# Kernel optimization log

Hardware: AMD Instinct MI355X
Metric: run time of the kernel (lower is better)

The kernel has to match this reference:

```python
import jax, jax.numpy as jnp
import numpy as np

N_QUBITS = 12
DIM = 2 ** N_QUBITS
BATCH = 2048


def setup_inputs() -> dict:
    key = jax.random.key(0)
    k1, k2, k3 = jax.random.split(key, 3)
    inputs = jax.random.normal(k1, (BATCH, N_QUBITS), dtype=jnp.float32)
    weight = jax.random.normal(k2, (3 + 2 * N_QUBITS,), dtype=jnp.float32)
    entangle_matrix = jax.random.normal(k3, (DIM, DIM), dtype=jnp.float32)
    return {"inputs": inputs, "weight": weight, "entangle_matrix": entangle_matrix}


def _encode(ry_angles, rz_angles):
    # Encoder: state = prod over qubits of first column of (Rz*Ry) per qubit.
    ry = ry_angles / 2
    rz = rz_angles / 2
    a = jnp.cos(ry) * jnp.exp(-1j * rz)  # entry11 (row bit = 0)
    b = jnp.sin(ry) * jnp.exp(1j * rz)   # entry21 (row bit = 1)
    col2 = jnp.stack([a, b], axis=-1).astype(jnp.complex64)  # [B, n, 2]
    B, n = ry.shape
    v = jnp.ones((B, 1), dtype=jnp.complex64)
    for q in range(n):  # Kronecker fold over qubits (big-endian, matches dec2bin)
        v = (v[:, :, None] * col2[:, q][:, None, :]).reshape(B, -1)
    return v  # [B, 2^n]


def _rot_mat(w):
    # rot_mat: per-qubit Rx(w[q]) @ Rz(w[n+q]), then full Kronecker product.
    n = w.shape[0] // 2
    tx = (w[:n] / 2).astype(jnp.complex64)
    tz = (w[n:] / 2).astype(jnp.complex64)
    c, s = jnp.cos(tx), jnp.sin(tx)
    rx = jnp.stack([jnp.stack([c, -1j * s], -1),
                    jnp.stack([-1j * s, c], -1)], -2)  # [n,2,2]
    ez = jnp.exp(-1j * tz)
    zero = jnp.zeros_like(ez)
    rz = jnp.stack([jnp.stack([ez, zero], -1),
                    jnp.stack([zero, jnp.exp(1j * tz)], -1)], -2)  # [n,2,2]
    mats = jnp.einsum('qij,qjk->qik', rx, rz)
    M = mats[0]
    for q in range(1, n):
        M = jnp.kron(M, mats[q])
    return M  # [2^n, 2^n]


def _ry2(theta):
    a = theta / 2
    c, s = jnp.cos(a), jnp.sin(a)
    return jnp.stack([jnp.stack([c, -s]), jnp.stack([s, c])])  # [2,2] real


def _final_rot(th3):
    # final_rot_mat: Rz-form @ Ry-form @ Rx-form (all ry_mat_list), kron with identity.
    rot = _ry2(th3[2]) @ (_ry2(th3[1]) @ _ry2(th3[0]))
    eye = jnp.eye(DIM // 2, dtype=jnp.complex64)
    return jnp.kron(rot.astype(jnp.complex64), eye)  # [DIM, DIM]


def reference(inputs, weight, entangle_matrix):
    # initial=False branch
    ry_angles = inputs
    rz_angles = jnp.square(inputs)
    v = _encode(ry_angles, rz_angles)                 # [B, DIM] complex64
    E = entangle_matrix.astype(jnp.complex64)
    R = _rot_mat(weight[3:])
    M = E @ R @ E                                     # [DIM, DIM]
    v = v @ M.T                                       # tensordot dims ([-1],[-1])
    F = _final_rot(weight[:3])
    v = v @ F.T
    half = DIM // 2
    # vector[:, half:] = 0 then sum |.|^2  <=>  sum over first half
    return jnp.sum(jnp.square(jnp.abs(v[:, :half])), axis=-1)  # [B] float32
```

## Files before the change

### kernel.cpp

```cpp
#include <hip/hip_runtime.h>
#include <math.h>

#define QDIM 4096
#define NQ 12
#define QBATCH 2048

typedef _Float16 f16x8 __attribute__((ext_vector_type(8)));
typedef float f32x4 __attribute__((ext_vector_type(4)));
typedef int i32x4 __attribute__((ext_vector_type(4)));

__device__ __forceinline__ void gld_lds16(const void* gptr, void* ldsptr) {
    __builtin_amdgcn_global_load_lds(
        (const __attribute__((address_space(1))) void*)gptr,
        (__attribute__((address_space(3))) void*)ldsptr,
        16, 0, 0);
}

__device__ __forceinline__ int q8(float x) {
    float y = fminf(fmaxf(x, -127.f), 127.f);
    return (int)rintf(y);
}
__device__ __forceinline__ int pack4_i8(int a, int b, int c, int d) {
    return (a & 0xFF) | ((b & 0xFF) << 8) | ((c & 0xFF) << 16) | ((d & 0xFF) << 24);
}

__global__ __launch_bounds__(256) void conv_kernel(
    const float* __restrict__ E, const float* __restrict__ wgt,
    _Float16* __restrict__ Eh, signed char* __restrict__ G8)
{
    float th = 0.5f * (wgt[0] + wgt[1] + wgt[2]);
    float c0 = cosf(th), c1 = -sinf(th);
    const float qs = 127.f / 6.f;
    size_t flat = ((size_t)blockIdx.x * 256 + threadIdx.x) * 8;
    size_t n = flat >> 12;
    size_t k = flat & (QDIM - 1);
    const float* p0 = E + n * QDIM + k;
    const float* p1 = p0 + (size_t)QBATCH * QDIM;
    float4 a0 = ((const float4*)p0)[0], a1 = ((const float4*)p0)[1];
    float4 b0 = ((const float4*)p1)[0], b1 = ((const float4*)p1)[1];
    f16x8 h0 = { (_Float16)a0.x, (_Float16)a0.y, (_Float16)a0.z, (_Float16)a0.w,
                 (_Float16)a1.x, (_Float16)a1.y, (_Float16)a1.z, (_Float16)a1.w };
    f16x8 h1 = { (_Float16)b0.x, (_Float16)b0.y, (_Float16)b0.z, (_Float16)b0.w,
                 (_Float16)b1.x, (_Float16)b1.y, (_Float16)b1.z, (_Float16)b1.w };
    *(f16x8*)&Eh[n * QDIM + k] = h0;
    *(f16x8*)&Eh[(n + QBATCH) * QDIM + k] = h1;
    float g[8] = { c0*a0.x + c1*b0.x, c0*a0.y + c1*b0.y, c0*a0.z + c1*b0.z, c0*a0.w + c1*b0.w,
                   c0*a1.x + c1*b1.x, c0*a1.y + c1*b1.y, c0*a1.z + c1*b1.z, c0*a1.w + c1*b1.w };
    int2 gp = { pack4_i8(q8(g[0]*qs), q8(g[1]*qs), q8(g[2]*qs), q8(g[3]*qs)),
                pack4_i8(q8(g[4]*qs), q8(g[5]*qs), q8(g[6]*qs), q8(g[7]*qs)) };
    *(int2*)&G8[n * QDIM + k] = gp;
}

__global__ __launch_bounds__(256) void expand_kernel(
    const float* __restrict__ inputs, _Float16* __restrict__ A1,
    float* __restrict__ out)
{
    __shared__ float ab[NQ][4];
    const int b = blockIdx.x;
    const int tid = threadIdx.x;
    if (tid == 0) out[b] = 0.f;
    if (tid < NQ) {
        float x = inputs[b * NQ + tid];
        float ry = 0.5f * x;
        float rz = 0.5f * x * x;
        float ca = cosf(ry), sa = sinf(ry), cz = cosf(rz), sz = sinf(rz);
        ab[tid][0] = ca * cz;  ab[tid][1] = -ca * sz;
        ab[tid][2] = sa * cz;  ab[tid][3] =  sa * sz;
    }
    __syncthreads();
    float pr0 = 1.f, pi0 = 0.f;
#pragma unroll
    for (int q = 0; q < 8; ++q) {
        int bit = (tid >> (7 - q)) & 1;
        float cr = ab[q][bit * 2 + 0], ci = ab[q][bit * 2 + 1];
        float nr = pr0 * cr - pi0 * ci;
        float ni = pr0 * ci + pi0 * cr;
        pr0 = nr; pi0 = ni;
    }
    f16x8 vr[2], vi[2];
#pragma unroll
    for (int u = 0; u < 16; ++u) {
        float pr = pr0, pi = pi0;
#pragma unroll
        for (int q = 8; q < 12; ++q) {
            int bit = (u >> (11 - q)) & 1;
            float cr = ab[q][bit * 2 + 0], ci = ab[q][bit * 2 + 1];
            float nr = pr * cr - pi * ci;
            float ni = pr * ci + pi * cr;
            pr = nr; pi = ni;
        }
        vr[u >> 3][u & 7] = (_Float16)pr;
        vi[u >> 3][u & 7] = (_Float16)pi;
    }
    const int idx0 = tid * 16;
    *(f16x8*)&A1[(size_t)b * QDIM + idx0] = vr[0];
    *(f16x8*)&A1[(size_t)b * QDIM + idx0 + 8] = vr[1];
    *(f16x8*)&A1[(size_t)(b + QBATCH) * QDIM + idx0] = vi[0];
    *(f16x8*)&A1[(size_t)(b + QBATCH) * QDIM + idx0 + 8] = vi[1];
}

#define VMCNT(N_) asm volatile("s_waitcnt vmcnt(" #N_ ")" ::: "memory")
#define LGKM0()   asm volatile("s_waitcnt lgkmcnt(0)" ::: "memory")
#define LGKM8()   asm volatile("s_waitcnt lgkmcnt(8)" ::: "memory")
#define SBAR()                              \
    do {                                    \
        asm volatile("" ::: "memory");      \
        __builtin_amdgcn_s_barrier();       \
        asm volatile("" ::: "memory");      \
    } while (0)

__global__ __launch_bounds__(512, 2) void gemm_f16_256(
    const _Float16* __restrict__ A, const _Float16* __restrict__ B,
    _Float16* __restrict__ C, int N)
{
    const int K = QDIM;
    __shared__ __attribute__((aligned(16))) _Float16 As[2][256 * 64];
    __shared__ __attribute__((aligned(16))) _Float16 Bs[2][256 * 64];

    const int tid  = threadIdx.x;
    const int wave = tid >> 6;
    const int lane = tid & 63;
    const int bm0 = blockIdx.y * 256;
    const int bn0 = blockIdx.x * 256;
    const int wm0 = (wave >> 2) * 128;
    const int wn0 = (wave & 3) * 64;
    const int q = lane >> 4;
    const int r = lane & 15;
    const int rx = r & 7;

    f32x4 acc[8][4];
#pragma unroll
    for (int i = 0; i < 8; ++i)
#pragma unroll
        for (int j = 0; j < 4; ++j) acc[i][j] = (f32x4){0.f, 0.f, 0.f, 0.f};

    const int srow = tid >> 3;
    const int scol = ((tid & 7) ^ (srow & 7)) * 8;
    const _Float16* gA = A + (size_t)(bm0 + srow) * K + scol;
    const _Float16* gB = B + (size_t)(bn0 + srow) * K + scol;

#define STG_A(D, KK, NN) gld_lds16(gA + (size_t)(NN) * 64 * K + (KK), &As[D][(NN) * 4096 + wave * 512])
#define STG_B(D, KK, NN) gld_lds16(gB + (size_t)(NN) * 64 * K + (KK), &Bs[D][(NN) * 4096 + wave * 512])
#define STG_AH(D, KK, H) do { STG_A(D, KK, 2*(H)); STG_A(D, KK, 2*(H)+1); } while (0)
#define STG_BH(D, KK, H) do { STG_B(D, KK, 2*(H)); STG_B(D, KK, 2*(H)+1); } while (0)

#define RD_A4(DST, D, IB)                                                          \
    _Pragma("unroll")                                                              \
    for (int ii = 0; ii < 4; ++ii) {                                               \
        _Pragma("unroll")                                                          \
        for (int ss = 0; ss < 2; ++ss)                                             \
            DST[ii][ss] = *(const f16x8*)&As[D][(wm0 + ((IB) + ii) * 16 + r) * 64  \
                                                + (((ss * 4 + q) ^ rx) * 8)];      \
    }
#define RD_B2(DST, D, JB)                                                          \
    _Pragma("unroll")                                                              \
    for (int jj = 0; jj < 2; ++jj) {                                               \
        _Pragma("unroll")                                                          \
        for (int ss = 0; ss < 2; ++ss)                                             \
            DST[jj][ss] = *(const f16x8*)&Bs[D][(wn0 + ((JB) + jj) * 16 + r) * 64  \
                                                + (((ss * 4 + q) ^ rx) * 8)];      \
    }
#define MM8(AR, BR, I0, J0)                                                        \
    _Pragma("unroll")                                                              \
    for (int ii = 0; ii < 4; ++ii) {                                               \
        _Pragma("unroll")                                                          \
        for (int jj = 0; jj < 2; ++jj) {                                           \
            acc[(I0) + ii][(J0) + jj] = __builtin_amdgcn_mfma_f32_16x16x32_f16(    \
                AR[ii][0], BR[jj][0], acc[(I0) + ii][(J0) + jj], 0, 0, 0);         \
            acc[(I0) + ii][(J0) + jj] = __builtin_amdgcn_mfma_f32_16x16x32_f16(    \
                AR[ii][1], BR[jj][1], acc[(I0) + ii][(J0) + jj], 0, 0, 0);         \
        }                                                                          \
    }

    f16x8 a0[4][2], a1[4][2], b0[2][2], b1[2][2];

    STG_AH(0, 0, 0); STG_AH(0, 0, 1);
    STG_BH(0, 0, 0); STG_BH(0, 0, 1);
    STG_BH(1, 64, 0); STG_BH(1, 64, 1);
    VMCNT(4);
    SBAR();

    for (int tau = 0; tau < 32; ++tau) {
        const int k1 = (2 * tau + 1) * 64;
        const int k2 = ((2 * tau + 2) & 63) * 64;
        const int k3 = ((2 * tau + 3) & 63) * 64;

        RD_A4(a0, 0, 0); RD_B2(b0, 0, 0);
        STG_AH(1, k1, 0);
        LGKM8();
        SBAR(); LGKM0();
        __builtin_amdgcn_s_setprio(1);
        MM8(a0, b0, 0, 0);
        __builtin_amdgcn_s_setprio(0);
        SBAR();

        RD_B2(b1, 0, 2);
        STG_AH(1, k1, 1);
        SBAR(); LGKM0();
        __builtin_amdgcn_s_setprio(1);
        MM8(a0, b1, 0, 2);
        __builtin_amdgcn_s_setprio(0);
        SBAR();

        RD_A4(a1, 0, 4);
        STG_BH(0, k2, 0);
        SBAR(); LGKM0();
        __builtin_amdgcn_s_setprio(1);
        MM8(a1, b1, 4, 2);
        __builtin_amdgcn_s_setprio(0);
        SBAR();

        STG_BH(0, k2, 1);
        VMCNT(4);
        SBAR(); LGKM0();
        __builtin_amdgcn_s_setprio(1);
        MM8(a1, b0, 4, 0);
        __builtin_amdgcn_s_setprio(0);
        SBAR();

        RD_A4(a0, 1, 0); RD_B2(b0, 1, 0);
        STG_AH(0, k2, 0);
        LGKM8();
        SBAR(); LGKM0();
        __builtin_amdgcn_s_setprio(1);
        MM8(a0, b0, 0, 0);
        __builtin_amdgcn_s_setprio(0);
        SBAR();

        RD_B2(b1, 1, 2);
        STG_AH(0, k2, 1);
        SBAR(); LGKM0();
        __builtin_amdgcn_s_setprio(1);
        MM8(a0, b1, 0, 2);
        __builtin_amdgcn_s_setprio(0);
        SBAR();

        RD_A4(a1, 1, 4);
        STG_BH(1, k3, 0);
        SBAR(); LGKM0();
        __builtin_amdgcn_s_setprio(1);
        MM8(a1, b1, 4, 2);
        __builtin_amdgcn_s_setprio(0);
        SBAR();

        STG_BH(1, k3, 1);
        VMCNT(4);
        SBAR(); LGKM0();
        __builtin_amdgcn_s_setprio(1);
        MM8(a1, b0, 4, 0);
        __builtin_amdgcn_s_setprio(0);
        SBAR();
    }
    VMCNT(0);

#pragma unroll
    for (int i = 0; i < 8; ++i) {
        const int crow = bm0 + wm0 + i * 16 + q * 4;
#pragma unroll
        for (int rr = 0; rr < 4; ++rr)
#pragma unroll
            for (int j = 0; j < 4; ++j)
                C[(size_t)(crow + rr) * N + bn0 + wn0 + j * 16 + r] = (_Float16)acc[i][j][rr];
    }
#undef STG_A
#undef STG_B
#undef STG_AH
#undef STG_BH
#undef RD_A4
#undef RD_B2
#undef MM8
}

__global__ __launch_bounds__(256) void butterfly_kernel(
    const _Float16* __restrict__ u1, const float* __restrict__ wgt,
    signed char* __restrict__ A2, float* __restrict__ scaleA)
{
    __shared__ float sRe[4366];
    __shared__ float sIm[4366];
    __shared__ float mats[NQ][8];
    __shared__ float red[8];
    const int blk = blockIdx.x;
    const int tid = threadIdx.x;
    const int ah = tid >> 4;
    const int al = tid & 15;

    if (tid < NQ) {
        float tx = 0.5f * wgt[3 + tid];
        float tz = 0.5f * wgt[15 + tid];
        float c = cosf(tx), s = sinf(tx), cz = cosf(tz), sz = sinf(tz);
        mats[tid][0] =  c * cz;  mats[tid][1] = -c * sz;
        mats[tid][2] =  s * sz;  mats[tid][3] = -s * cz;
        mats[tid][4] = -s * sz;  mats[tid][5] = -s * cz;
        mats[tid][6] =  c * cz;  mats[tid][7] =  c * sz;
    }

    float xr[16], xi[16];
    {
        const _Float16* pRe = u1 + (size_t)blk * QDIM + tid * 16;
        const _Float16* pIm = u1 + (size_t)(blk + QBATCH) * QDIM + tid * 16;
        f16x8 r0 = ((const f16x8*)pRe)[0], r1 = ((const f16x8*)pRe)[1];
        f16x8 i0 = ((const f16x8*)pIm)[0], i1 = ((const f16x8*)pIm)[1];
#pragma unroll
        for (int j = 0; j < 8; ++j) {
            xr[j] = (float)r0[j]; xr[8 + j] = (float)r1[j];
            xi[j] = (float)i0[j]; xi[8 + j] = (float)i1[j];
        }
    }
    __syncthreads();

#define BFLY_STAGE(arrR, arrI, K_, Q_)                                         \
    {                                                                          \
        const float m00r = mats[Q_][0], m00i = mats[Q_][1];                    \
        const float m01r = mats[Q_][2], m01i = mats[Q_][3];                    \
        const float m10r = mats[Q_][4], m10i = mats[Q_][5];                    \
        const float m11r = mats[Q_][6], m11i = mats[Q_][7];                    \
        _Pragma("unroll")                                                      \
        for (int t = 0; t < 8; ++t) {                                          \
            int i0 = ((t >> (K_)) << ((K_) + 1)) | (t & ((1 << (K_)) - 1));    \
            int i1 = i0 | (1 << (K_));                                         \
            float x0r = arrR[i0], x0i = arrI[i0];                              \
            float x1r = arrR[i1], x1i = arrI[i1];                              \
            arrR[i0] = m00r * x0r - m00i * x0i + m01r * x1r - m01i * x1i;      \
            arrI[i0] = m00r * x0i + m00i * x0r + m01r * x1i + m01i * x1r;      \
            arrR[i1] = m10r * x0r - m10i * x0i + m11r * x1r - m11i * x1i;      \
            arrI[i1] = m10r * x0i + m10i * x0r + m11r * x1i + m11i * x1r;      \
        }                                                                      \
    }

#pragma unroll
    for (int p = 0; p < 4; ++p) BFLY_STAGE(xr, xi, p, 11 - p);

#pragma unroll
    for (int c = 0; c < 16; ++c) {
        sRe[273 * ah + 17 * al + c] = xr[c];
        sIm[273 * ah + 17 * al + c] = xi[c];
    }
    __syncthreads();

    float yr[16], yi[16];
#pragma unroll
    for (int b = 0; b < 16; ++b) {
        yr[b] = sRe[273 * ah + 17 * b + al];
        yi[b] = sIm[273 * ah + 17 * b + al];
    }
#pragma unroll
    for (int p = 0; p < 4; ++p) BFLY_STAGE(yr, yi, p, 7 - p);

#pragma unroll
    for (int b = 0; b < 16; ++b) {
        sRe[273 * ah + 17 * b + al] = yr[b];
        sIm[273 * ah + 17 * b + al] = yi[b];
    }
    __syncthreads();

    float zr[16], zi[16];
#pragma unroll
    for (int a = 0; a < 16; ++a) {
        zr[a] = sRe[273 * a + 17 * ah + al];
        zi[a] = sIm[273 * a + 17 * ah + al];
    }
#pragma unroll
    for (int p = 0; p < 4; ++p) BFLY_STAGE(zr, zi, p, 3 - p);

    float mR = 0.f, mI = 0.f;
#pragma unroll
    for (int j = 0; j < 16; ++j) {
        mR = fmaxf(mR, fabsf(zr[j]));
        mI = fmaxf(mI, fabsf(zi[j]));
    }
#pragma unroll
    for (int off = 32; off > 0; off >>= 1) {
        mR = fmaxf(mR, __shfl_xor(mR, off, 64));
        mI = fmaxf(mI, __shfl_xor(mI, off, 64));
    }
    const int wid = tid >> 6;
    if ((tid & 63) == 0) { red[wid] = mR; red[4 + wid] = mI; }
    __syncthreads();
    mR = fmaxf(fmaxf(red[0], red[1]), fmaxf(red[2], red[3]));
    mI = fmaxf(fmaxf(red[4], red[5]), fmaxf(red[6], red[7]));
    mR = fmaxf(mR, 1e-30f);
    mI = fmaxf(mI, 1e-30f);
    if (tid == 0) {
        scaleA[blk] = mR / 127.f;
        scaleA[blk + QBATCH] = mI / 127.f;
    }
    const float invR = 127.f / mR, invI = 127.f / mI;

    signed char* oRe = A2 + (size_t)blk * QDIM + ah * 16 + al;
    signed char* oIm = A2 + (size_t)(blk + QBATCH) * QDIM + ah * 16 + al;
#pragma unroll
    for (int a = 0; a < 16; ++a) {
        oRe[a * 256] = (signed char)q8(zr[a] * invR);
        oIm[a * 256] = (signed char)q8(zi[a] * invI);
    }
#undef BFLY_STAGE
}

__global__ __launch_bounds__(256) void gemm2_i8(
    const signed char* __restrict__ A, const signed char* __restrict__ B,
    const float* __restrict__ scaleA, float* __restrict__ out)
{
    const int K = QDIM;
    __shared__ __attribute__((aligned(16))) signed char As[128 * 128];
    __shared__ __attribute__((aligned(16))) signed char Bs[128 * 128];

    const int tid  = threadIdx.x;
    const int wave = tid >> 6;
    const int lane = tid & 63;
    const int bn0 = blockIdx.x * 128;
    const int bm0 = blockIdx.y * 128;
    const int wm = (wave >> 1) * 64;
    const int wn = (wave & 1) * 64;
    const int q = lane >> 4;
    const int r = lane & 15;
    const int rx = r & 7;

    i32x4 acc[4][4];
#pragma unroll
    for (int i = 0; i < 4; ++i)
#pragma unroll
        for (int j = 0; j < 4; ++j) acc[i][j] = (i32x4){0, 0, 0, 0};

    const signed char* gA[4];
    const signed char* gB[4];
    char* lA[4];
    char* lB[4];
#pragma unroll
    for (int n = 0; n < 4; ++n) {
        int c = n * 256 + tid;
        int row = c >> 3;
        int gcol = (c & 7) ^ (row & 7);
        gA[n] = A + (size_t)(bm0 + row) * K + gcol * 16;
        gB[n] = B + (size_t)(bn0 + row) * K + gcol * 16;
        lA[n] = (char*)As + (n * 256 + wave * 64) * 16;
        lB[n] = (char*)Bs + (n * 256 + wave * 64) * 16;
    }

    for (int kk = 0; kk < K; kk += 128) {
#pragma unroll
        for (int n = 0; n < 4; ++n) {
            gld_lds16(gA[n] + kk, lA[n]);
            gld_lds16(gB[n] + kk, lB[n]);
        }
        __syncthreads();

#pragma unroll
        for (int s = 0; s < 2; ++s) {
            i32x4 af[4], bf[4];
#pragma unroll
            for (int i = 0; i < 4; ++i) {
                int row = wm + i * 16 + r;
                af[i] = *(const i32x4*)&As[row * 128 + (((s * 4 + q) ^ rx) * 16)];
            }
#pragma unroll
            for (int j = 0; j < 4; ++j) {
                int row = wn + j * 16 + r;
                bf[j] = *(const i32x4*)&Bs[row * 128 + (((s * 4 + q) ^ rx) * 16)];
            }
#pragma unroll
            for (int i = 0; i < 4; ++i)
#pragma unroll
                for (int j = 0; j < 4; ++j)
                    acc[i][j] = __builtin_amdgcn_mfma_i32_16x16x64_i8(af[i], bf[j], acc[i][j], 0, 0, 0);
        }
        __syncthreads();
    }

    const float dqG = 6.f / 127.f;
#pragma unroll
    for (int i = 0; i < 4; ++i) {
#pragma unroll
        for (int rr = 0; rr < 4; ++rr) {
            const int row = bm0 + wm + i * 16 + q * 4 + rr;
            const float sc = scaleA[row] * dqG;
            float v = 0.f;
#pragma unroll
            for (int j = 0; j < 4; ++j) {
                float t = sc * (float)acc[i][j][rr];
                v = fmaf(t, t, v);
            }
            v += __shfl_xor(v, 1, 64);
            v += __shfl_xor(v, 2, 64);
            v += __shfl_xor(v, 4, 64);
            v += __shfl_xor(v, 8, 64);
            if (r == 0) atomicAdd(&out[row & (QBATCH - 1)], v);
        }
    }
}

extern "C" void kernel_launch(void* const* d_in, const int* in_sizes, int n_in,
                              void* d_out, int out_size, void* d_ws, size_t ws_size,
                              hipStream_t stream)
{
    const float* inputs = (const float*)d_in[0];
    const float* weight = (const float*)d_in[1];
    const float* E      = (const float*)d_in[2];
    float* out = (float*)d_out;

    char* ws = (char*)d_ws;
    const size_t MB = 1024 * 1024;
    _Float16*    Eh     = (_Float16*)   (ws + 0);
    signed char* G8     = (signed char*)(ws + 32 * MB);
    _Float16*    A1     = (_Float16*)   (ws + 40 * MB);
    _Float16*    u1     = (_Float16*)   (ws + 72 * MB);
    signed char* A2     = (signed char*)(ws + 104 * MB);
    float*       scaleA = (float*)      (ws + 120 * MB);

    conv_kernel<<<(QBATCH * QDIM / 8) / 256, 256, 0, stream>>>(E, weight, Eh, G8);
    expand_kernel<<<QBATCH, 256, 0, stream>>>(inputs, A1, out);
    gemm_f16_256<<<dim3(QDIM / 256, QDIM / 256), 512, 0, stream>>>(A1, Eh, u1, QDIM);
    butterfly_kernel<<<QBATCH, 256, 0, stream>>>(u1, weight, A2, scaleA);
    gemm2_i8<<<dim3(2048 / 128, QDIM / 128), 256, 0, stream>>>(A2, G8, scaleA, out);
}
```

Measured before the change: 299.0 us.

## Software-pipeline LDS fragment reads one phase ahead of MFMA blocks

Moves each LDS fragment read so it is issued right after the barrier and overlaps the MFMA block of the current phase, with an extra b0n register set for double buffering. It also reorders the A staging halves and loosens vmcnt waits so global-to-LDS loads have more slack. The goal is to hide LDS read latency behind matrix math. In exchange it uses more registers, which could hurt occupancy at launch_bounds(512,2), and the reworked wait counts risk race conditions if they are wrong.

```diff
diff --git a/kernel.cpp b/kernel.cpp
--- a/kernel.cpp
+++ b/kernel.cpp
@@ -101,7 +101,7 @@
 
 #define VMCNT(N_) asm volatile("s_waitcnt vmcnt(" #N_ ")" ::: "memory")
 #define LGKM0()   asm volatile("s_waitcnt lgkmcnt(0)" ::: "memory")
-#define LGKM8()   asm volatile("s_waitcnt lgkmcnt(8)" ::: "memory")
+#define SCHED0()  __builtin_amdgcn_sched_barrier(0)
 #define SBAR()                              \
     do {                                    \
         asm volatile("" ::: "memory");      \
@@ -141,7 +141,7 @@
 
 #define STG_A(D, KK, NN) gld_lds16(gA + (size_t)(NN) * 64 * K + (KK), &As[D][(NN) * 4096 + wave * 512])
 #define STG_B(D, KK, NN) gld_lds16(gB + (size_t)(NN) * 64 * K + (KK), &Bs[D][(NN) * 4096 + wave * 512])
-#define STG_AH(D, KK, H) do { STG_A(D, KK, 2*(H)); STG_A(D, KK, 2*(H)+1); } while (0)
+#define STG_AH(D, KK, H) do { STG_A(D, KK, (H)); STG_A(D, KK, 2 + (H)); } while (0)
 #define STG_BH(D, KK, H) do { STG_B(D, KK, 2*(H)); STG_B(D, KK, 2*(H)+1); } while (0)
 
 #define RD_A4(DST, D, IB)                                                          \
@@ -172,82 +172,88 @@
         }                                                                          \
     }
 
-    f16x8 a0[4][2], a1[4][2], b0[2][2], b1[2][2];
-
+    f16x8 a0[4][2], a1[4][2], b0[2][2], b0n[2][2], b1[2][2];
+
+    STG_BH(0, 0, 0); STG_BH(0, 0, 1);
     STG_AH(0, 0, 0); STG_AH(0, 0, 1);
-    STG_BH(0, 0, 0); STG_BH(0, 0, 1);
     STG_BH(1, 64, 0); STG_BH(1, 64, 1);
-    VMCNT(4);
+    VMCNT(6);
     SBAR();
+    RD_A4(a0, 0, 0);
+    RD_B2(b0, 0, 0);
 
     for (int tau = 0; tau < 32; ++tau) {
         const int k1 = (2 * tau + 1) * 64;
         const int k2 = ((2 * tau + 2) & 63) * 64;
         const int k3 = ((2 * tau + 3) & 63) * 64;
 
-        RD_A4(a0, 0, 0); RD_B2(b0, 0, 0);
         STG_AH(1, k1, 0);
-        LGKM8();
-        SBAR(); LGKM0();
+        SBAR(); LGKM0(); SCHED0();
+        RD_B2(b1, 0, 2);
         __builtin_amdgcn_s_setprio(1);
         MM8(a0, b0, 0, 0);
         __builtin_amdgcn_s_setprio(0);
         SBAR();
 
-        RD_B2(b1, 0, 2);
         STG_AH(1, k1, 1);
-        SBAR(); LGKM0();
+        VMCNT(8);
+        SBAR(); LGKM0(); SCHED0();
+        RD_A4(a1, 0, 4);
         __builtin_amdgcn_s_setprio(1);
         MM8(a0, b1, 0, 2);
         __builtin_amdgcn_s_setprio(0);
         SBAR();
 
-        RD_A4(a1, 0, 4);
         STG_BH(0, k2, 0);
-        SBAR(); LGKM0();
+        VMCNT(6);
+        SBAR(); LGKM0(); SCHED0();
+        RD_B2(b0n, 1, 0);
         __builtin_amdgcn_s_setprio(1);
         MM8(a1, b1, 4, 2);
         __builtin_amdgcn_s_setprio(0);
         SBAR();
 
         STG_BH(0, k2, 1);
-        VMCNT(4);
-        SBAR(); LGKM0();
+        VMCNT(6);
+        SBAR(); LGKM0(); SCHED0();
+        RD_A4(a0, 1, 0);
         __builtin_amdgcn_s_setprio(1);
         MM8(a1, b0, 4, 0);
         __builtin_amdgcn_s_setprio(0);
         SBAR();
 
-        RD_A4(a0, 1, 0); RD_B2(b0, 1, 0);
         STG_AH(0, k2, 0);
-        LGKM8();
-        SBAR(); LGKM0();
-        __builtin_amdgcn_s_setprio(1);
-        MM8(a0, b0, 0, 0);
-        __builtin_amdgcn_s_setprio(0);
-        SBAR();
-
+        SBAR(); LGKM0(); SCHED0();
         RD_B2(b1, 1, 2);
+        __builtin_amdgcn_s_setprio(1);
+        MM8(a0, b0n, 0, 0);
+        __builtin_amdgcn_s_setprio(0);
+        SBAR();
+
         STG_AH(0, k2, 1);
-        SBAR(); LGKM0();
+        VMCNT(8);
+        SBAR(); LGKM0(); SCHED0();
+        RD_A4(a1, 1, 4);
         __builtin_amdgcn_s_setprio(1);
         MM8(a0, b1, 0, 2);
         __builtin_amdgcn_s_setprio(0);
         SBAR();
 
-        RD_A4(a1, 1, 4);
         STG_BH(1, k3, 0);
-        SBAR(); LGKM0();
+        VMCNT(6);
+        SBAR(); LGKM0(); SCHED0();
+        RD_B2(b0, 0, 0);
         __builtin_amdgcn_s_setprio(1);
         MM8(a1, b1, 4, 2);
         __builtin_amdgcn_s_setprio(0);
         SBAR();
 
         STG_BH(1, k3, 1);
-        VMCNT(4);
-        SBAR(); LGKM0();
-        __builtin_amdgcn_s_setprio(1);
-        MM8(a1, b0, 4, 0);
+        VMCNT(6);
+        SBAR(); LGKM0(); SCHED0();
+        RD_A4(a0, 0, 0);
+        __builtin_amdgcn_s_setprio(1);
+        MM8(a1, b0n, 4, 0);
         __builtin_amdgcn_s_setprio(0);
         SBAR();
     }
```

Result: slower. 364.1 us (+21.8%).

## Restructure int8 GEMM2 into 256x128 tile with double-buffered ping-pong pipeline

Applied to the files above, without the earlier changes.

Replaces the 128x128, 256-thread int8 GEMM with a 256x128 tile run by 512 threads. It double-buffers LDS and interleaves async global-to-LDS loads with MFMA sub-blocks, using barriers, explicit vmcnt/lgkm waits and setprio, which is meant to hide load latency behind compute. The larger tile also halves B-tile reloads per A row. The cost is more LDS per block (96KB) and dependence on macros (VMCNT, SBAR, LGKM0) assumed to be defined earlier in the file.

```diff
diff --git a/kernel.cpp b/kernel.cpp
--- a/kernel.cpp
+++ b/kernel.cpp
@@ -396,21 +396,21 @@
 #undef BFLY_STAGE
 }
 
-__global__ __launch_bounds__(256) void gemm2_i8(
+__global__ __launch_bounds__(512, 2) void gemm2_i8_256(
     const signed char* __restrict__ A, const signed char* __restrict__ B,
     const float* __restrict__ scaleA, float* __restrict__ out)
 {
     const int K = QDIM;
-    __shared__ __attribute__((aligned(16))) signed char As[128 * 128];
-    __shared__ __attribute__((aligned(16))) signed char Bs[128 * 128];
+    __shared__ __attribute__((aligned(16))) signed char As[2][256 * 128];
+    __shared__ __attribute__((aligned(16))) signed char Bs[2][128 * 128];
 
     const int tid  = threadIdx.x;
     const int wave = tid >> 6;
     const int lane = tid & 63;
     const int bn0 = blockIdx.x * 128;
-    const int bm0 = blockIdx.y * 128;
-    const int wm = (wave >> 1) * 64;
-    const int wn = (wave & 1) * 64;
+    const int bm0 = blockIdx.y * 256;
+    const int wm0 = (wave >> 1) * 64;
+    const int wn0 = (wave & 1) * 64;
     const int q = lane >> 4;
     const int r = lane & 15;
     const int rx = r & 7;
@@ -421,57 +421,125 @@
 #pragma unroll
         for (int j = 0; j < 4; ++j) acc[i][j] = (i32x4){0, 0, 0, 0};
 
-    const signed char* gA[4];
-    const signed char* gB[4];
-    char* lA[4];
-    char* lB[4];
-#pragma unroll
-    for (int n = 0; n < 4; ++n) {
-        int c = n * 256 + tid;
-        int row = c >> 3;
-        int gcol = (c & 7) ^ (row & 7);
-        gA[n] = A + (size_t)(bm0 + row) * K + gcol * 16;
-        gB[n] = B + (size_t)(bn0 + row) * K + gcol * 16;
-        lA[n] = (char*)As + (n * 256 + wave * 64) * 16;
-        lB[n] = (char*)Bs + (n * 256 + wave * 64) * 16;
-    }
-
-    for (int kk = 0; kk < K; kk += 128) {
-#pragma unroll
-        for (int n = 0; n < 4; ++n) {
-            gld_lds16(gA[n] + kk, lA[n]);
-            gld_lds16(gB[n] + kk, lB[n]);
-        }
-        __syncthreads();
-
-#pragma unroll
-        for (int s = 0; s < 2; ++s) {
-            i32x4 af[4], bf[4];
-#pragma unroll
-            for (int i = 0; i < 4; ++i) {
-                int row = wm + i * 16 + r;
-                af[i] = *(const i32x4*)&As[row * 128 + (((s * 4 + q) ^ rx) * 16)];
-            }
-#pragma unroll
-            for (int j = 0; j < 4; ++j) {
-                int row = wn + j * 16 + r;
-                bf[j] = *(const i32x4*)&Bs[row * 128 + (((s * 4 + q) ^ rx) * 16)];
-            }
-#pragma unroll
-            for (int i = 0; i < 4; ++i)
-#pragma unroll
-                for (int j = 0; j < 4; ++j)
-                    acc[i][j] = __builtin_amdgcn_mfma_i32_16x16x64_i8(af[i], bf[j], acc[i][j], 0, 0, 0);
-        }
-        __syncthreads();
-    }
+    const int srow = tid >> 3;
+    const int scol = ((tid & 7) ^ (srow & 7)) * 16;
+    const signed char* gA = A + (size_t)(bm0 + srow) * K + scol;
+    const signed char* gB = B + (size_t)(bn0 + srow) * K + scol;
+
+#define STG2_A(D, KK, NN) gld_lds16(gA + (size_t)(NN) * 64 * K + (KK), &As[D][(NN) * 8192 + wave * 1024])
+#define STG2_B(D, KK, NN) gld_lds16(gB + (size_t)(NN) * 64 * K + (KK), &Bs[D][(NN) * 8192 + wave * 1024])
+
+#define RD2_A(DST, D, IB)                                                           \
+    _Pragma("unroll")                                                               \
+    for (int ii = 0; ii < 2; ++ii) {                                                \
+        _Pragma("unroll")                                                           \
+        for (int ss = 0; ss < 2; ++ss)                                              \
+            DST[ii][ss] = *(const i32x4*)&As[D][(wm0 + ((IB) + ii) * 16 + r) * 128  \
+                                                + (((ss * 4 + q) ^ rx) * 16)];      \
+    }
+#define RD2_B(DST, D, JB)                                                           \
+    _Pragma("unroll")                                                               \
+    for (int jj = 0; jj < 2; ++jj) {                                                \
+        _Pragma("unroll")                                                           \
+        for (int ss = 0; ss < 2; ++ss)                                              \
+            DST[jj][ss] = *(const i32x4*)&Bs[D][(wn0 + ((JB) + jj) * 16 + r) * 128  \
+                                                + (((ss * 4 + q) ^ rx) * 16)];      \
+    }
+#define MM2(AR, BR, I0, J0)                                                         \
+    _Pragma("unroll")                                                               \
+    for (int ii = 0; ii < 2; ++ii) {                                                \
+        _Pragma("unroll")                                                           \
+        for (int jj = 0; jj < 2; ++jj) {                                            \
+            acc[(I0) + ii][(J0) + jj] = __builtin_amdgcn_mfma_i32_16x16x64_i8(      \
+                AR[ii][0], BR[jj][0], acc[(I0) + ii][(J0) + jj], 0, 0, 0);          \
+            acc[(I0) + ii][(J0) + jj] = __builtin_amdgcn_mfma_i32_16x16x64_i8(      \
+                AR[ii][1], BR[jj][1], acc[(I0) + ii][(J0) + jj], 0, 0, 0);          \
+        }                                                                           \
+    }
+
+    i32x4 a0[2][2], a1[2][2], b0[2][2], b1[2][2];
+
+    STG2_B(0, 0, 0); STG2_B(0, 0, 1);
+    STG2_A(0, 0, 0); STG2_A(0, 0, 1); STG2_A(0, 0, 2); STG2_A(0, 0, 3);
+    STG2_B(1, 128, 0); STG2_B(1, 128, 1);
+    VMCNT(2);
+    SBAR();
+
+    for (int tau = 0; tau < 16; ++tau) {
+        const int k1 = (2 * tau + 1) * 128;
+        const int k2 = ((2 * tau + 2) & 31) * 128;
+        const int k3 = ((2 * tau + 3) & 31) * 128;
+
+        RD2_A(a0, 0, 0); RD2_B(b0, 0, 0);
+        STG2_A(1, k1, 0); STG2_A(1, k1, 1);
+        SBAR(); LGKM0();
+        __builtin_amdgcn_s_setprio(1);
+        MM2(a0, b0, 0, 0);
+        __builtin_amdgcn_s_setprio(0);
+        SBAR();
+
+        RD2_B(b1, 0, 2);
+        STG2_A(1, k1, 2); STG2_A(1, k1, 3);
+        SBAR(); LGKM0();
+        __builtin_amdgcn_s_setprio(1);
+        MM2(a0, b1, 0, 2);
+        __builtin_amdgcn_s_setprio(0);
+        SBAR();
+
+        RD2_A(a1, 0, 2);
+        SBAR(); LGKM0();
+        __builtin_amdgcn_s_setprio(1);
+        MM2(a1, b1, 2, 2);
+        __builtin_amdgcn_s_setprio(0);
+        SBAR();
+
+        STG2_B(0, k2, 0); STG2_B(0, k2, 1);
+        VMCNT(2);
+        SBAR(); LGKM0();
+        __builtin_amdgcn_s_setprio(1);
+        MM2(a1, b0, 2, 0);
+        __builtin_amdgcn_s_setprio(0);
+        SBAR();
+
+        RD2_A(a0, 1, 0); RD2_B(b0, 1, 0);
+        STG2_A(0, k2, 0); STG2_A(0, k2, 1);
+        SBAR(); LGKM0();
+        __builtin_amdgcn_s_setprio(1);
+        MM2(a0, b0, 0, 0);
+        __builtin_amdgcn_s_setprio(0);
+        SBAR();
+
+        RD2_B(b1, 1, 2);
+        STG2_A(0, k2, 2); STG2_A(0, k2, 3);
+        SBAR(); LGKM0();
+        __builtin_amdgcn_s_setprio(1);
+        MM2(a0, b1, 0, 2);
+        __builtin_amdgcn_s_setprio(0);
+        SBAR();
+
+        RD2_A(a1, 1, 2);
+        SBAR(); LGKM0();
+        __builtin_amdgcn_s_setprio(1);
+        MM2(a1, b1, 2, 2);
+        __builtin_amdgcn_s_setprio(0);
+        SBAR();
+
+        STG2_B(1, k3, 0); STG2_B(1, k3, 1);
+        VMCNT(2);
+        SBAR(); LGKM0();
+        __builtin_amdgcn_s_setprio(1);
+        MM2(a1, b0, 2, 0);
+        __builtin_amdgcn_s_setprio(0);
+        SBAR();
+    }
+    VMCNT(0);
 
     const float dqG = 6.f / 127.f;
 #pragma unroll
     for (int i = 0; i < 4; ++i) {
 #pragma unroll
         for (int rr = 0; rr < 4; ++rr) {
-            const int row = bm0 + wm + i * 16 + q * 4 + rr;
+            const int row = bm0 + wm0 + i * 16 + q * 4 + rr;
             const float sc = scaleA[row] * dqG;
             float v = 0.f;
 #pragma unroll
@@ -486,6 +554,11 @@
             if (r == 0) atomicAdd(&out[row & (QBATCH - 1)], v);
         }
     }
+#undef STG2_A
+#undef STG2_B
+#undef RD2_A
+#undef RD2_B
+#undef MM2
 }
 
 extern "C" void kernel_launch(void* const* d_in, const int* in_sizes, int n_in,
@@ -510,5 +583,5 @@
     expand_kernel<<<QBATCH, 256, 0, stream>>>(inputs, A1, out);
     gemm_f16_256<<<dim3(QDIM / 256, QDIM / 256), 512, 0, stream>>>(A1, Eh, u1, QDIM);
     butterfly_kernel<<<QBATCH, 256, 0, stream>>>(u1, weight, A2, scaleA);
-    gemm2_i8<<<dim3(2048 / 128, QDIM / 128), 256, 0, stream>>>(A2, G8, scaleA, out);
-}
+    gemm2_i8_256<<<dim3(2048 / 128, QDIM / 256), 512, 0, stream>>>(A2, G8, scaleA, out);
+}
```

Result: no change. 298.1 us (-0.3%).
